# Optimization experiments

Hardware: AMD Instinct MI355X
Metric: run time of the kernel (lower is better)

The kernel has to match this reference:

```python
import jax, jax.numpy as jnp
import numpy as np

K = 4096  # num_embeddings
D = 256   # embedding_dim

def setup_inputs() -> dict:
    key = jax.random.key(0)
    k1, k2 = jax.random.split(key)
    z_e = jax.random.normal(k1, (32, 32, 32, 256), dtype=jnp.float32)
    embedding = jax.random.normal(k2, (K, D), dtype=jnp.float32)
    return {"z_e": z_e, "embedding": embedding}

def reference(z_e, embedding):
    # z_e: [B,H,W,D] channels-last; embedding: [K,D]
    B, H, W, Dd = z_e.shape
    z_flat = z_e.reshape(-1, Dd)                                   # [N,D]
    # squared L2 distances via expansion: ||z||^2 + ||e||^2 - 2 z.e
    distances = (jnp.sum(z_flat**2, axis=1, keepdims=True)
                 + jnp.sum(embedding**2, axis=1)
                 - 2.0 * jnp.matmul(z_flat, embedding.T))          # [N,K]
    indices = jnp.argmin(distances, axis=1)                        # [N]
    z_q = embedding[indices].reshape(B, H, W, Dd)                  # gather
    # straight-through estimator
    z_q = z_e + jax.lax.stop_gradient(z_q - z_e)
    # perplexity (codebook utilization)
    avg_probs = jnp.bincount(indices, length=K).astype(jnp.float32) / indices.shape[0]
    perplexity = jnp.exp(-jnp.sum(avg_probs * jnp.log(avg_probs + 1e-10)))
    return z_q, indices.reshape(B, H, W), perplexity
```

## Files before the change

kernel.cpp:

```cpp
#include <hip/hip_runtime.h>
#include <hip/hip_bf16.h>
#include <math.h>
#include <stdint.h>

typedef _Float16 f16;
typedef _Float16 f16x8 __attribute__((ext_vector_type(8)));
typedef float f32x16 __attribute__((ext_vector_type(16)));

#define DIM 256
#define LOSCALE 2048.0f
#define INV_LOSCALE (1.0f/2048.0f)

#define BP_BYTES (4096u*1024u + 32768u)

#define GLOAD16(gp, lp) __builtin_amdgcn_global_load_lds( \
    (const __attribute__((address_space(1))) void*)(gp),  \
    (__attribute__((address_space(3))) void*)(lp), 16, 0, 0)

__global__ void vq_pack2(const float* __restrict__ emb, f16* __restrict__ bp)
{
    int o = blockIdx.x * blockDim.x + threadIdx.x;
    int l = o & 63;
    int b = o >> 6;
    int t   = b & 1;
    int s   = (b >> 1) & 15;
    int col = b >> 5;
    int code  = col * 32 + (l & 31);
    int depth = s * 16 + (l >> 5) * 8;
    const float* gp = emb + (size_t)code * DIM + depth;
    float4 x0 = *(const float4*)gp;
    float4 x1 = *(const float4*)(gp + 4);
    float xs[8] = {x0.x, x0.y, x0.z, x0.w, x1.x, x1.y, x1.z, x1.w};
    f16x8 v;
    #pragma unroll
    for (int j = 0; j < 8; ++j) {
        f16 h = (f16)xs[j];
        v[j] = t ? (f16)((xs[j] - (float)h) * LOSCALE) : h;
    }
    *(f16x8*)(bp + (size_t)o * 8) = v;
}

__global__ void vq_e2(const float* __restrict__ emb, float* __restrict__ e2) {
    int k = blockIdx.x;
    int l = threadIdx.x;
    float4 v = ((const float4*)(emb + (size_t)k * DIM))[l];
    float s = v.x * v.x + v.y * v.y + v.z * v.z + v.w * v.w;
    #pragma unroll
    for (int off = 32; off; off >>= 1) s += __shfl_xor(s, off);
    if (l == 0) e2[k] = s;
}

__global__ void vq_zero(int* __restrict__ p, int n) {
    int i = blockIdx.x * blockDim.x + threadIdx.x;
    if (i < n) p[i] = 0;
}

__global__ __launch_bounds__(256, 2) void vq_argmin7(
    const float* __restrict__ z, const char* __restrict__ bp,
    const float* __restrict__ e2, unsigned long long* __restrict__ part)
{
    __shared__ __align__(16) char bufs[4][16384];
    __shared__ float e2s[2048];

    const int t    = threadIdx.x;
    const int lane = t & 63;
    const int rt   = t >> 6;
    const int hw   = blockIdx.x & 1;
    const int rg   = blockIdx.x >> 1;
    const int l31  = lane & 31;
    const int hi5  = lane >> 5;
    const int rowbase = rg * 128 + rt * 32;

    *(float4*)&e2s[t * 8]     = *(const float4*)(e2 + hw * 2048 + t * 8);
    *(float4*)&e2s[t * 8 + 4] = *(const float4*)(e2 + hw * 2048 + t * 8 + 4);

    f16x8 a_h[16], a_l[16];
    {
        const float* zr = z + (size_t)(rowbase + l31) * DIM + hi5 * 8;
        #pragma unroll
        for (int s = 0; s < 16; ++s) {
            float4 x0 = *(const float4*)(zr + s * 16);
            float4 x1 = *(const float4*)(zr + s * 16 + 4);
            float xs[8] = {x0.x, x0.y, x0.z, x0.w, x1.x, x1.y, x1.z, x1.w};
            #pragma unroll
            for (int j = 0; j < 8; ++j) {
                f16 h = (f16)xs[j];
                a_h[s][j] = h;
                a_l[s][j] = (f16)((xs[j] - (float)h) * LOSCALE);
            }
        }
    }
    __syncthreads();

    float    bestd[16];
    unsigned bcol[4];
    #pragma unroll
    for (int q = 0; q < 16; ++q) bestd[q] = 3.4e38f;
    #pragma unroll
    for (int i = 0; i < 4; ++i) bcol[i] = 0u;

    const char* bhalf = bp + ((size_t)hw << 21);

#define STAGE(pb, uu) do {                                                    \
    const char* src_ = bhalf + ((size_t)(uu) << 14) + (size_t)t * 16;         \
    char* dst_ = bufs[pb] + t * 16;                                           \
    _Pragma("unroll")                                                         \
    for (int i_ = 0; i_ < 4; ++i_)                                            \
        GLOAD16(src_ + i_ * 4096, dst_ + i_ * 4096);                          \
    } while (0)

#define COMPUTE8(BB, SB) do {                                                 \
    const char* bbp_ = (BB);                                                  \
    f16x8 bh_ = *(const f16x8*)(bbp_ + lane * 16);                            \
    f16x8 bl_ = *(const f16x8*)(bbp_ + 1024 + lane * 16);                     \
    __builtin_amdgcn_s_setprio(1);                                            \
    _Pragma("unroll")                                                         \
    for (int sl_ = 0; sl_ < 8; ++sl_) {                                       \
        f16x8 bhn_, bln_;                                                     \
        if (sl_ < 7) {                                                        \
            bhn_ = *(const f16x8*)(bbp_ + (sl_+1) * 2048 + lane * 16);        \
            bln_ = *(const f16x8*)(bbp_ + (sl_+1) * 2048 + 1024 + lane * 16); \
        }                                                                     \
        acc0  = __builtin_amdgcn_mfma_f32_32x32x16_f16(a_h[(SB)+sl_], bh_, acc0,  0,0,0); \
        acc1a = __builtin_amdgcn_mfma_f32_32x32x16_f16(a_h[(SB)+sl_], bl_, acc1a, 0,0,0); \
        acc1b = __builtin_amdgcn_mfma_f32_32x32x16_f16(a_l[(SB)+sl_], bh_, acc1b, 0,0,0); \
        if (sl_ < 7) { bh_ = bhn_; bl_ = bln_; }                              \
    }                                                                         \
    __builtin_amdgcn_s_setprio(0);                                            \
    } while (0)

#define PHASE_SYNC() do {                                                     \
    asm volatile("s_waitcnt vmcnt(8)" ::: "memory");                          \
    asm volatile("s_waitcnt lgkmcnt(0)" ::: "memory");                        \
    __builtin_amdgcn_s_barrier();                                             \
    __builtin_amdgcn_sched_barrier(0);                                        \
    } while (0)

    STAGE(0, 0);
    STAGE(1, 1);

    for (int c = 0; c < 64; ++c) {
        float e2c = e2s[c * 32 + l31];
        f32x16 acc0, acc1a, acc1b;
        #pragma unroll
        for (int q = 0; q < 16; ++q) { acc0[q] = 0.0f; acc1a[q] = 0.0f; acc1b[q] = 0.0f; }

        STAGE((2*c + 2) & 3, 2*c + 2);
        PHASE_SYNC();
        COMPUTE8(bufs[(2*c) & 3], 0);

        STAGE((2*c + 3) & 3, 2*c + 3);
        PHASE_SYNC();
        COMPUTE8(bufs[(2*c + 1) & 3], 8);

        #pragma unroll
        for (int q = 0; q < 16; ++q) {
            float dot  = fmaf(acc1a[q] + acc1b[q], INV_LOSCALE, acc0[q]);
            float dist = fmaf(-2.0f, dot, e2c);
            bool  lt   = dist < bestd[q];
            bestd[q]   = lt ? dist : bestd[q];
            const unsigned sh = (unsigned)((q & 3) * 8);
            unsigned nv = (bcol[q >> 2] & ~(0xFFu << sh)) | ((unsigned)c << sh);
            bcol[q >> 2] = lt ? nv : bcol[q >> 2];
        }
    }
#undef STAGE
#undef COMPUTE8
#undef PHASE_SYNC

    #pragma unroll
    for (int q = 0; q < 16; ++q) {
        float    d = bestd[q];
        unsigned c = (unsigned)(hw * 2048) +
                     ((bcol[q >> 2] >> ((q & 3) * 8)) & 0xFFu) * 32u + (unsigned)l31;
        #pragma unroll
        for (int o2 = 16; o2; o2 >>= 1) {
            float    od = __shfl_xor(d, o2);
            unsigned oc = __shfl_xor(c, o2);
            if (od < d || (od == d && oc < c)) { d = od; c = oc; }
        }
        if (l31 == 0) {
            int row = (q & 3) + 8 * (q >> 2) + 4 * hi5;
            unsigned u   = __float_as_uint(d);
            unsigned key = u ^ (unsigned)(((int)u >> 31) | 0x80000000);
            part[(size_t)hw * 32768 + rowbase + row] =
                ((unsigned long long)key << 32) | c;
        }
    }
}

__global__ void vq_combine(const unsigned long long* __restrict__ part,
                           float* __restrict__ idxf, int N)
{
    int i = blockIdx.x * blockDim.x + threadIdx.x;
    if (i >= N) return;
    unsigned long long a = part[i];
    unsigned long long b = part[(size_t)N + i];
    unsigned long long m = b < a ? b : a;
    idxf[i] = (float)(unsigned)(m & 0xffffffffu);
}

__global__ __launch_bounds__(256, 2) void vq_argmin_f32(
    const float* __restrict__ z, const float* __restrict__ emb,
    const float* __restrict__ e2, float* __restrict__ idxf, int K)
{
    __shared__ float zs[64 * 36];
    __shared__ float es[128 * 36];
    const int t = threadIdx.x;
    const int tx = t & 15;
    const int ty = t >> 4;
    const int rowbase = blockIdx.x * 64;
    const float* zbase = z + (size_t)rowbase * DIM;
    float best[4]; int bidx[4];
    #pragma unroll
    for (int i = 0; i < 4; ++i) { best[i] = 3.4e38f; bidx[i] = 0; }
    for (int kt = 0; kt < K; kt += 128) {
        float acc[4][8];
        #pragma unroll
        for (int i = 0; i < 4; ++i)
            #pragma unroll
            for (int j = 0; j < 8; ++j) acc[i][j] = 0.0f;
        for (int dc = 0; dc < DIM; dc += 32) {
            { int lr = t >> 2, o = (t & 3) * 8;
              const float* gp = zbase + (size_t)lr * DIM + dc + o;
              *(float4*)&zs[lr*36+o]   = *(const float4*)gp;
              *(float4*)&zs[lr*36+o+4] = *(const float4*)(gp+4); }
            { int lc = t >> 1, o = (t & 1) * 16;
              const float* gp = emb + (size_t)(kt+lc) * DIM + dc + o;
              *(float4*)&es[lc*36+o]    = *(const float4*)gp;
              *(float4*)&es[lc*36+o+4]  = *(const float4*)(gp+4);
              *(float4*)&es[lc*36+o+8]  = *(const float4*)(gp+8);
              *(float4*)&es[lc*36+o+12] = *(const float4*)(gp+12); }
            __syncthreads();
            const float* zp = &zs[(ty*4)*36];
            const float* ep = &es[tx*36];
            #pragma unroll
            for (int d = 0; d < 32; d += 4) {
                float4 zv[4], ev[8];
                #pragma unroll
                for (int i = 0; i < 4; ++i) zv[i] = *(const float4*)&zp[i*36+d];
                #pragma unroll
                for (int j = 0; j < 8; ++j) ev[j] = *(const float4*)&ep[j*16*36+d];
                #pragma unroll
                for (int i = 0; i < 4; ++i)
                    #pragma unroll
                    for (int j = 0; j < 8; ++j) {
                        acc[i][j] += zv[i].x*ev[j].x; acc[i][j] += zv[i].y*ev[j].y;
                        acc[i][j] += zv[i].z*ev[j].z; acc[i][j] += zv[i].w*ev[j].w;
                    }
            }
            __syncthreads();
        }
        #pragma unroll
        for (int j = 0; j < 8; ++j) {
            int c = kt + tx + 16*j;
            float ev2 = e2[c];
            #pragma unroll
            for (int i = 0; i < 4; ++i) {
                float dist = ev2 - 2.0f*acc[i][j];
                if (dist < best[i] || (dist == best[i] && c < bidx[i])) { best[i]=dist; bidx[i]=c; }
            }
        }
    }
    #pragma unroll
    for (int i = 0; i < 4; ++i) {
        float bd = best[i]; int bi = bidx[i];
        #pragma unroll
        for (int off = 8; off; off >>= 1) {
            float od = __shfl_xor(bd, off); int oi = __shfl_xor(bi, off);
            if (od < bd || (od == bd && oi < bi)) { bd = od; bi = oi; }
        }
        if (tx == 0) idxf[rowbase + ty*4 + i] = (float)bi;
    }
}

__global__ void vq_gather(const float* __restrict__ emb,
                          const float* __restrict__ idxf,
                          float* __restrict__ zq, int N)
{
    int n = blockIdx.x * 4 + (threadIdx.x >> 6);
    int l = threadIdx.x & 63;
    if (n >= N) return;
    int idx = (int)idxf[n];
    ((float4*)(zq + (size_t)n * DIM))[l] = ((const float4*)(emb + (size_t)idx * DIM))[l];
}

__global__ void vq_hist(const float* __restrict__ idxf, int* __restrict__ counts, int N) {
    int n = blockIdx.x * blockDim.x + threadIdx.x;
    if (n < N) atomicAdd(&counts[(int)idxf[n]], 1);
}

__global__ void vq_ppl(const int* __restrict__ counts, float invN,
                       float* __restrict__ out, int K)
{
    int t = threadIdx.x;
    float s = 0.0f;
    for (int k = t; k < K; k += 256) {
        float p = (float)counts[k] * invN;
        s += p * logf(p + 1e-10f);
    }
    #pragma unroll
    for (int off = 32; off; off >>= 1) s += __shfl_xor(s, off);
    __shared__ float wsum[4];
    if ((t & 63) == 0) wsum[t >> 6] = s;
    __syncthreads();
    if (t == 0) out[0] = expf(-(wsum[0] + wsum[1] + wsum[2] + wsum[3]));
}

extern "C" void kernel_launch(void* const* d_in, const int* in_sizes, int n_in,
                              void* d_out, int out_size, void* d_ws, size_t ws_size,
                              hipStream_t stream)
{
    const float* z   = (const float*)d_in[0];
    const float* emb = (const float*)d_in[1];
    const int N = in_sizes[0] / DIM;
    const int K = in_sizes[1] / DIM;

    float* out  = (float*)d_out;
    float* zq   = out;
    float* idxf = out + (size_t)N * DIM;
    float* ppl  = idxf + N;

    const size_t PART_BYTES = 2ull * 32768 * sizeof(unsigned long long);
    const size_t NEED = (size_t)BP_BYTES + 16384 + 16384 + PART_BYTES;

    if (ws_size >= NEED && K == 4096 && N == 32768) {
        f16*   bpk    = (f16*)d_ws;
        float* e2     = (float*)((char*)d_ws + BP_BYTES);
        int*   counts = (int*)((char*)d_ws + BP_BYTES + 16384);
        unsigned long long* part =
            (unsigned long long*)((char*)d_ws + BP_BYTES + 32768);

        vq_pack2<<<1024, 256, 0, stream>>>(emb, bpk);
        vq_e2<<<K, 64, 0, stream>>>(emb, e2);
        vq_zero<<<(K + 255) / 256, 256, 0, stream>>>(counts, K);
        vq_argmin7<<<(N / 128) * 2, 256, 0, stream>>>(z, (const char*)bpk, e2, part);
        vq_combine<<<N / 256, 256, 0, stream>>>(part, idxf, N);
        vq_gather<<<N / 4, 256, 0, stream>>>(emb, idxf, zq, N);
        vq_hist<<<(N + 255) / 256, 256, 0, stream>>>(idxf, counts, N);
        vq_ppl<<<1, 256, 0, stream>>>(counts, 1.0f / (float)N, ppl, K);
    } else {
        float* e2     = (float*)d_ws;
        int*   counts = (int*)((char*)d_ws + (size_t)K * sizeof(float));
        vq_e2<<<K, 64, 0, stream>>>(emb, e2);
        vq_zero<<<(K + 255) / 256, 256, 0, stream>>>(counts, K);
        vq_argmin_f32<<<N / 64, 256, 0, stream>>>(z, emb, e2, idxf, K);
        vq_gather<<<N / 4, 256, 0, stream>>>(emb, idxf, zq, N);
        vq_hist<<<(N + 255) / 256, 256, 0, stream>>>(idxf, counts, N);
        vq_ppl<<<1, 256, 0, stream>>>(counts, 1.0f / (float)N, ppl, K);
    }
}
```

Measured before the change: 241.0 us.

## Process two 32-row tiles per wave to reuse each codebook fragment twice

Each wave now holds A fragments for 64 rows instead of 32, so every B fragment read from LDS feeds two row tiles. This halves LDS reads and global codebook streaming per row, and halves the grid. The two correction MFMAs are chained into a single accumulator, which saves one accumulator per tile. Register pressure roughly doubles for the A fragments (launch bounds drop to 1 block per SM), which lowers occupancy and leaves fewer blocks to spread across CUs.

```diff
diff --git a/kernel.cpp b/kernel.cpp
--- a/kernel.cpp
+++ b/kernel.cpp
@@ -55,7 +55,7 @@
     if (i < n) p[i] = 0;
 }
 
-__global__ __launch_bounds__(256, 2) void vq_argmin7(
+__global__ __launch_bounds__(256, 1) void vq_argmin8(
     const float* __restrict__ z, const char* __restrict__ bp,
     const float* __restrict__ e2, unsigned long long* __restrict__ part)
 {
@@ -69,35 +69,42 @@
     const int rg   = blockIdx.x >> 1;
     const int l31  = lane & 31;
     const int hi5  = lane >> 5;
-    const int rowbase = rg * 128 + rt * 32;
+    const int rowbase = rg * 256 + rt * 64;
 
     *(float4*)&e2s[t * 8]     = *(const float4*)(e2 + hw * 2048 + t * 8);
     *(float4*)&e2s[t * 8 + 4] = *(const float4*)(e2 + hw * 2048 + t * 8 + 4);
 
-    f16x8 a_h[16], a_l[16];
+    f16x8 a_h0[16], a_l0[16], a_h1[16], a_l1[16];
     {
-        const float* zr = z + (size_t)(rowbase + l31) * DIM + hi5 * 8;
+        const float* zr0 = z + (size_t)(rowbase + l31) * DIM + hi5 * 8;
+        const float* zr1 = z + (size_t)(rowbase + 32 + l31) * DIM + hi5 * 8;
         #pragma unroll
         for (int s = 0; s < 16; ++s) {
-            float4 x0 = *(const float4*)(zr + s * 16);
-            float4 x1 = *(const float4*)(zr + s * 16 + 4);
+            float4 x0 = *(const float4*)(zr0 + s * 16);
+            float4 x1 = *(const float4*)(zr0 + s * 16 + 4);
+            float4 y0 = *(const float4*)(zr1 + s * 16);
+            float4 y1 = *(const float4*)(zr1 + s * 16 + 4);
             float xs[8] = {x0.x, x0.y, x0.z, x0.w, x1.x, x1.y, x1.z, x1.w};
+            float ys[8] = {y0.x, y0.y, y0.z, y0.w, y1.x, y1.y, y1.z, y1.w};
             #pragma unroll
             for (int j = 0; j < 8; ++j) {
-                f16 h = (f16)xs[j];
-                a_h[s][j] = h;
-                a_l[s][j] = (f16)((xs[j] - (float)h) * LOSCALE);
+                f16 h0 = (f16)xs[j];
+                a_h0[s][j] = h0;
+                a_l0[s][j] = (f16)((xs[j] - (float)h0) * LOSCALE);
+                f16 h1 = (f16)ys[j];
+                a_h1[s][j] = h1;
+                a_l1[s][j] = (f16)((ys[j] - (float)h1) * LOSCALE);
             }
         }
     }
     __syncthreads();
 
-    float    bestd[16];
-    unsigned bcol[4];
-    #pragma unroll
-    for (int q = 0; q < 16; ++q) bestd[q] = 3.4e38f;
-    #pragma unroll
-    for (int i = 0; i < 4; ++i) bcol[i] = 0u;
+    float    bestd0[16], bestd1[16];
+    unsigned bc0[4], bc1[4];
+    #pragma unroll
+    for (int q = 0; q < 16; ++q) { bestd0[q] = 3.4e38f; bestd1[q] = 3.4e38f; }
+    #pragma unroll
+    for (int i = 0; i < 4; ++i) { bc0[i] = 0u; bc1[i] = 0u; }
 
     const char* bhalf = bp + ((size_t)hw << 21);
 
@@ -121,9 +128,12 @@
             bhn_ = *(const f16x8*)(bbp_ + (sl_+1) * 2048 + lane * 16);        \
             bln_ = *(const f16x8*)(bbp_ + (sl_+1) * 2048 + 1024 + lane * 16); \
         }                                                                     \
-        acc0  = __builtin_amdgcn_mfma_f32_32x32x16_f16(a_h[(SB)+sl_], bh_, acc0,  0,0,0); \
-        acc1a = __builtin_amdgcn_mfma_f32_32x32x16_f16(a_h[(SB)+sl_], bl_, acc1a, 0,0,0); \
-        acc1b = __builtin_amdgcn_mfma_f32_32x32x16_f16(a_l[(SB)+sl_], bh_, acc1b, 0,0,0); \
+        acc0_0 = __builtin_amdgcn_mfma_f32_32x32x16_f16(a_h0[(SB)+sl_], bh_, acc0_0, 0,0,0); \
+        acc0_1 = __builtin_amdgcn_mfma_f32_32x32x16_f16(a_h1[(SB)+sl_], bh_, acc0_1, 0,0,0); \
+        f32x16 t0_ = __builtin_amdgcn_mfma_f32_32x32x16_f16(a_h0[(SB)+sl_], bl_, acc1_0, 0,0,0); \
+        f32x16 t1_ = __builtin_amdgcn_mfma_f32_32x32x16_f16(a_h1[(SB)+sl_], bl_, acc1_1, 0,0,0); \
+        acc1_0 = __builtin_amdgcn_mfma_f32_32x32x16_f16(a_l0[(SB)+sl_], bh_, t0_, 0,0,0); \
+        acc1_1 = __builtin_amdgcn_mfma_f32_32x32x16_f16(a_l1[(SB)+sl_], bh_, t1_, 0,0,0); \
         if (sl_ < 7) { bh_ = bhn_; bl_ = bln_; }                              \
     }                                                                         \
     __builtin_amdgcn_s_setprio(0);                                            \
@@ -140,10 +150,11 @@
     STAGE(1, 1);
 
     for (int c = 0; c < 64; ++c) {
-        float e2c = e2s[c * 32 + l31];
-        f32x16 acc0, acc1a, acc1b;
-        #pragma unroll
-        for (int q = 0; q < 16; ++q) { acc0[q] = 0.0f; acc1a[q] = 0.0f; acc1b[q] = 0.0f; }
+        f32x16 acc0_0, acc0_1, acc1_0, acc1_1;
+        #pragma unroll
+        for (int q = 0; q < 16; ++q) {
+            acc0_0[q] = 0.0f; acc0_1[q] = 0.0f; acc1_0[q] = 0.0f; acc1_1[q] = 0.0f;
+        }
 
         STAGE((2*c + 2) & 3, 2*c + 2);
         PHASE_SYNC();
@@ -153,15 +164,22 @@
         PHASE_SYNC();
         COMPUTE8(bufs[(2*c + 1) & 3], 8);
 
+        float e2c = e2s[c * 32 + l31];
         #pragma unroll
         for (int q = 0; q < 16; ++q) {
-            float dot  = fmaf(acc1a[q] + acc1b[q], INV_LOSCALE, acc0[q]);
-            float dist = fmaf(-2.0f, dot, e2c);
-            bool  lt   = dist < bestd[q];
-            bestd[q]   = lt ? dist : bestd[q];
             const unsigned sh = (unsigned)((q & 3) * 8);
-            unsigned nv = (bcol[q >> 2] & ~(0xFFu << sh)) | ((unsigned)c << sh);
-            bcol[q >> 2] = lt ? nv : bcol[q >> 2];
+            float dot0  = fmaf(acc1_0[q], INV_LOSCALE, acc0_0[q]);
+            float dist0 = fmaf(-2.0f, dot0, e2c);
+            bool  lt0   = dist0 < bestd0[q];
+            bestd0[q]   = lt0 ? dist0 : bestd0[q];
+            unsigned nv0 = (bc0[q >> 2] & ~(0xFFu << sh)) | ((unsigned)c << sh);
+            bc0[q >> 2]  = lt0 ? nv0 : bc0[q >> 2];
+            float dot1  = fmaf(acc1_1[q], INV_LOSCALE, acc0_1[q]);
+            float dist1 = fmaf(-2.0f, dot1, e2c);
+            bool  lt1   = dist1 < bestd1[q];
+            bestd1[q]   = lt1 ? dist1 : bestd1[q];
+            unsigned nv1 = (bc1[q >> 2] & ~(0xFFu << sh)) | ((unsigned)c << sh);
+            bc1[q >> 2]  = lt1 ? nv1 : bc1[q >> 2];
         }
     }
 #undef STAGE
@@ -169,22 +187,26 @@
 #undef PHASE_SYNC
 
     #pragma unroll
-    for (int q = 0; q < 16; ++q) {
-        float    d = bestd[q];
-        unsigned c = (unsigned)(hw * 2048) +
-                     ((bcol[q >> 2] >> ((q & 3) * 8)) & 0xFFu) * 32u + (unsigned)l31;
-        #pragma unroll
-        for (int o2 = 16; o2; o2 >>= 1) {
-            float    od = __shfl_xor(d, o2);
-            unsigned oc = __shfl_xor(c, o2);
-            if (od < d || (od == d && oc < c)) { d = od; c = oc; }
-        }
-        if (l31 == 0) {
-            int row = (q & 3) + 8 * (q >> 2) + 4 * hi5;
-            unsigned u   = __float_as_uint(d);
-            unsigned key = u ^ (unsigned)(((int)u >> 31) | 0x80000000);
-            part[(size_t)hw * 32768 + rowbase + row] =
-                ((unsigned long long)key << 32) | c;
+    for (int m = 0; m < 2; ++m) {
+        #pragma unroll
+        for (int q = 0; q < 16; ++q) {
+            float    d = m ? bestd1[q] : bestd0[q];
+            unsigned cc = m ? ((bc1[q >> 2] >> ((q & 3) * 8)) & 0xFFu)
+                            : ((bc0[q >> 2] >> ((q & 3) * 8)) & 0xFFu);
+            unsigned c = (unsigned)(hw * 2048) + cc * 32u + (unsigned)l31;
+            #pragma unroll
+            for (int o2 = 16; o2; o2 >>= 1) {
+                float    od = __shfl_xor(d, o2);
+                unsigned oc = __shfl_xor(c, o2);
+                if (od < d || (od == d && oc < c)) { d = od; c = oc; }
+            }
+            if (l31 == 0) {
+                int row = (q & 3) + 8 * (q >> 2) + 4 * hi5 + m * 32;
+                unsigned u   = __float_as_uint(d);
+                unsigned key = u ^ (unsigned)(((int)u >> 31) | 0x80000000);
+                part[(size_t)hw * 32768 + rowbase + row] =
+                    ((unsigned long long)key << 32) | c;
+            }
         }
     }
 }
@@ -334,7 +356,7 @@
         vq_pack2<<<1024, 256, 0, stream>>>(emb, bpk);
         vq_e2<<<K, 64, 0, stream>>>(emb, e2);
         vq_zero<<<(K + 255) / 256, 256, 0, stream>>>(counts, K);
-        vq_argmin7<<<(N / 128) * 2, 256, 0, stream>>>(z, (const char*)bpk, e2, part);
+        vq_argmin8<<<(N / 256) * 2, 256, 0, stream>>>(z, (const char*)bpk, e2, part);
         vq_combine<<<N / 256, 256, 0, stream>>>(part, idxf, N);
         vq_gather<<<N / 4, 256, 0, stream>>>(emb, idxf, zq, N);
         vq_hist<<<(N + 255) / 256, 256, 0, stream>>>(idxf, counts, N);
```

Result: slower. 247.5 us (+2.7%).
